# Kernel tuning notes

Hardware: AMD Instinct MI355X
Metric: run time of the kernel (lower is better)

Reference implementation:

```python
import jax, jax.numpy as jnp
import numpy as np

B, QS, KS, E, H = 2, 2048, 2048, 2048, 16
D = E // H  # head_dim = 128
EPS = 1e-6


def setup_inputs() -> dict:
    key = jax.random.key(0)
    ks = jax.random.split(key, 11)
    scale_in = 1.0 / np.sqrt(E)  # lecun_normal fan_in = E
    scale_out = 1.0 / np.sqrt(E)  # fan_in for out proj = H*D = E
    return {
        "q": jax.random.normal(ks[0], (B, QS, E), jnp.float32),
        "kv": jax.random.normal(ks[1], (B, KS, E), jnp.float32),
        "q_pos": jax.random.normal(ks[2], (B, QS, E), jnp.float32),
        "kv_pos": jax.random.normal(ks[3], (B, KS, E), jnp.float32),
        "mask": jax.random.bernoulli(ks[4], 0.5, (B, QS, KS)),
        "wq": jax.random.normal(ks[5], (E, H, D), jnp.float32) * scale_in,
        "wk": jax.random.normal(ks[6], (E, H, D), jnp.float32) * scale_in,
        "wv": jax.random.normal(ks[7], (E, H, D), jnp.float32) * scale_in,
        "q_ln_scale": jnp.ones((D,), jnp.float32),
        "k_ln_scale": jnp.ones((D,), jnp.float32),
        "wo": jax.random.normal(ks[8], (H, D, E), jnp.float32) * scale_out,
    }


def _layernorm_no_bias(x, scale):
    # flax LayerNorm over last axis, use_bias=False, epsilon=1e-6
    mu = jnp.mean(x, axis=-1, keepdims=True)
    var = jnp.mean(jnp.square(x - mu), axis=-1, keepdims=True)
    return (x - mu) * jax.lax.rsqrt(var + EPS) * scale


def reference(q, kv, q_pos, kv_pos, mask, wq, wk, wv, q_ln_scale, k_ln_scale, wo):
    dtype = q.dtype
    qi = q + q_pos          # [b, qs, e]
    ki = kv + kv_pos        # [b, ks, e]
    vi = kv
    # QKV projections (DenseGeneral, no bias) -> [b, s, h, d]
    qh = jnp.einsum('bqe,ehd->bqhd', qi, wq)
    kh = jnp.einsum('bke,ehd->bkhd', ki, wk)
    vh = jnp.einsum('bke,ehd->bkhd', vi, wv)
    # normalize_qk: LayerNorm (no bias) on query/key over head_dim
    qh = _layernorm_no_bias(qh, q_ln_scale)
    kh = _layernorm_no_bias(kh, k_ln_scale)
    # scaled dot-product with float32 logits
    qh = qh / jnp.sqrt(jnp.asarray(D, dtype))
    logits = jnp.einsum('bqhd,bkhd->bhqk', qh, kh,
                        preferred_element_type=jnp.float32)
    big_neg = jnp.finfo(jnp.float32).min
    logits = jnp.where(mask[:, None, :, :], logits, big_neg)
    attn = jax.nn.softmax(logits, axis=-1).astype(dtype)  # [b,h,q,k]
    out = jnp.einsum('bhqk,bkhd->bqhd', attn, vh)
    # output projection (DenseGeneral over (h,d), no bias)
    return jnp.einsum('bqhd,hde->bqe', out, wo)
```

## Files before the change

### kernel.cpp

```cpp
#include <hip/hip_runtime.h>
#include <hip/hip_bf16.h>


typedef __attribute__((ext_vector_type(8))) __bf16 bf16x8;
typedef __attribute__((ext_vector_type(4))) float f32x4;
typedef __attribute__((ext_vector_type(16))) float f32x16;
typedef __attribute__((ext_vector_type(8))) unsigned short ushort8;
typedef __attribute__((ext_vector_type(4))) unsigned short ushort4v;
typedef __attribute__((ext_vector_type(4))) unsigned uint4v;
typedef __attribute__((ext_vector_type(4))) float float4v;

#define MFMA16(a, b, c) __builtin_amdgcn_mfma_f32_16x16x32_bf16((a), (b), (c), 0, 0, 0)
#define MFMA32(a, b, c) __builtin_amdgcn_mfma_f32_32x32x16_bf16((a), (b), (c), 0, 0, 0)

__device__ __forceinline__ unsigned short f2bf(float f) {
  unsigned u = __builtin_bit_cast(unsigned, f);
  u += 0x7fffu + ((u >> 16) & 1u);
  return (unsigned short)(u >> 16);
}

__device__ __forceinline__ unsigned pkbf(float lo, float hi) {
  unsigned d;
  asm("v_cvt_pk_bf16_f32 %0, %1, %2" : "=v"(d) : "v"(lo), "v"(hi));
  return d;
}

__device__ __forceinline__ float max3f(float a, float b, float c) {
  float d;
  asm("v_max3_f32 %0, %1, %2, %3" : "=v"(d) : "v"(a), "v"(b), "v"(c));
  return d;
}

__device__ __forceinline__ float exp2a(float x) {
  float d;
  asm("v_exp_f32 %0, %1" : "=v"(d) : "v"(x));
  return d;
}

__device__ __forceinline__ void gload_lds16(const void* g, void* l) {
  __builtin_amdgcn_global_load_lds(
      (const __attribute__((address_space(1))) void*)g,
      (__attribute__((address_space(3))) void*)l, 16, 0, 0);
}

__global__ __launch_bounds__(256) void k_cvt(const float4v* __restrict__ x,
                                             const float4v* __restrict__ y,
                                             ushort4v* __restrict__ o, int n4) {
  int i = blockIdx.x * 256 + threadIdx.x;
  if (i >= n4) return;
  float4v a = x[i];
  if (y) { float4v b = y[i]; a = a + b; }
  ushort4v r;
  r[0] = f2bf(a[0]); r[1] = f2bf(a[1]); r[2] = f2bf(a[2]); r[3] = f2bf(a[3]);
  o[i] = r;
}

__global__ __launch_bounds__(256) void k_cvt2(const float4v* __restrict__ x,
                                              const float4v* __restrict__ y,
                                              ushort4v* __restrict__ oa,
                                              ushort4v* __restrict__ ob, int n4) {
  int i = blockIdx.x * 256 + threadIdx.x;
  if (i >= n4) return;
  float4v a = x[i];
  float4v s = a + y[i];
  ushort4v ra, rb;
  ra[0] = f2bf(s[0]); ra[1] = f2bf(s[1]); ra[2] = f2bf(s[2]); ra[3] = f2bf(s[3]);
  rb[0] = f2bf(a[0]); rb[1] = f2bf(a[1]); rb[2] = f2bf(a[2]); rb[3] = f2bf(a[3]);
  oa[i] = ra; ob[i] = rb;
}

__global__ __launch_bounds__(256) void k_tr(const float* __restrict__ s0, const float* __restrict__ s1,
                                            const float* __restrict__ s2, const float* __restrict__ s3,
                                            unsigned short* __restrict__ d0, unsigned short* __restrict__ d1,
                                            unsigned short* __restrict__ d2, unsigned short* __restrict__ d3) {
  __shared__ float t[32][33];
  const float* S; unsigned short* D;
  switch (blockIdx.z) {
    case 0: S = s0; D = d0; break;
    case 1: S = s1; D = d1; break;
    case 2: S = s2; D = d2; break;
    default: S = s3; D = d3; break;
  }
  int x = threadIdx.x & 31, y = threadIdx.x >> 5;
  int r0 = blockIdx.y * 32, c0 = blockIdx.x * 32;
#pragma unroll
  for (int i = 0; i < 4; ++i) t[y + 8 * i][x] = S[(size_t)(r0 + y + 8 * i) * 2048 + c0 + x];
  __syncthreads();
#pragma unroll
  for (int i = 0; i < 4; ++i)
    D[(size_t)(c0 + y + 8 * i) * 2048 + r0 + x] = f2bf(t[x][y + 8 * i]);
}

__global__ __launch_bounds__(256) void k_mask(const int* __restrict__ m,
                                              unsigned long long* __restrict__ out) {
  int i = blockIdx.x * 256 + threadIdx.x;
  unsigned long long b = __ballot(m[i] != 0);
  if ((threadIdx.x & 63) == 0) out[i >> 6] = b;
}

__global__ __launch_bounds__(256) void k_trv(const unsigned short* __restrict__ Vh,
                                             unsigned short* __restrict__ Vt) {
  __shared__ unsigned short t[64][72];
  int bh = blockIdx.z;
  int s0 = blockIdx.x * 64, d0 = blockIdx.y * 64;
  size_t base = (size_t)bh * 2048 * 128;
  int row = threadIdx.x >> 2, c16 = (threadIdx.x & 3) * 16;
  {
    const unsigned short* src = Vh + base + (size_t)(s0 + row) * 128 + d0 + c16;
    ushort8 a0 = *(const ushort8*)src;
    ushort8 a1 = *(const ushort8*)(src + 8);
#pragma unroll
    for (int e = 0; e < 8; ++e) {
      t[c16 + e][row] = a0[e];
      t[c16 + 8 + e][row] = a1[e];
    }
  }
  __syncthreads();
  {
    const int P0[8] = {0, 1, 2, 3, 8, 9, 10, 11};
    const int P1[8] = {4, 5, 6, 7, 12, 13, 14, 15};
    unsigned short* dst = Vt + base + (size_t)(d0 + row) * 2048 + s0 + c16;
    ushort8 w0, w1;
#pragma unroll
    for (int e = 0; e < 8; ++e) {
      w0[e] = t[row][c16 + P0[e]];
      w1[e] = t[row][c16 + P1[e]];
    }
    *(ushort8*)dst = w0;
    *(ushort8*)(dst + 8) = w1;
  }
}

template <int MODE>
__global__ __launch_bounds__(256) void k_gemm(const unsigned short* __restrict__ A,
                                              const unsigned short* __restrict__ Bt,
                                              void* __restrict__ Cv,
                                              const float* __restrict__ lnsc) {
  constexpr int K = 2048;
  __shared__ __attribute__((aligned(16))) unsigned short sA[128 * 64];
  __shared__ __attribute__((aligned(16))) unsigned short sB[128 * 64];
  __shared__ float sSum[2][128];
  __shared__ float sSq[2][128];
  int tid = threadIdx.x;
  int lane = tid & 63, w = tid >> 6;
  int wr = w >> 1, wc = w & 1;
  int r15 = lane & 15, blk = lane >> 4;
  int n0 = blockIdx.x * 128, m0 = blockIdx.y * 128;
  const unsigned short* Abase = A + (size_t)m0 * K;
  const unsigned short* Bbase = Bt + (size_t)n0 * K;
  f32x4 acc[4][4] = {};

  for (int kt = 0; kt < K; kt += 64) {
#pragma unroll
    for (int i = 0; i < 4; ++i) {
      int c = i * 256 + tid;
      int row = c >> 3, cc = c & 7;
      gload_lds16(Abase + (size_t)row * K + kt + ((cc ^ (row & 7)) * 8), &sA[c * 8]);
    }
#pragma unroll
    for (int i = 0; i < 4; ++i) {
      int c = i * 256 + tid;
      int row = c >> 3, cc = c & 7;
      gload_lds16(Bbase + (size_t)row * K + kt + ((cc ^ (row & 7)) * 8), &sB[c * 8]);
    }
    __syncthreads();
#pragma unroll
    for (int kk = 0; kk < 2; ++kk) {
      bf16x8 av[4], bv[4];
#pragma unroll
      for (int i = 0; i < 4; ++i) {
        int row = wr * 64 + i * 16 + r15;
        av[i] = *(const bf16x8*)&sA[row * 64 + (((kk * 4 + blk) ^ (row & 7)) * 8)];
      }
#pragma unroll
      for (int j = 0; j < 4; ++j) {
        int row = wc * 64 + j * 16 + r15;
        bv[j] = *(const bf16x8*)&sB[row * 64 + (((kk * 4 + blk) ^ (row & 7)) * 8)];
      }
#pragma unroll
      for (int i = 0; i < 4; ++i)
#pragma unroll
        for (int j = 0; j < 4; ++j) acc[i][j] = MFMA16(av[i], bv[j], acc[i][j]);
    }
    __syncthreads();
  }

  if constexpr (MODE == 3) {
    float* C = (float*)Cv;
#pragma unroll
    for (int i = 0; i < 4; ++i)
#pragma unroll
      for (int r = 0; r < 4; ++r)
#pragma unroll
        for (int j = 0; j < 4; ++j) {
          int rowl = wr * 64 + i * 16 + blk * 4 + r;
          int coll = wc * 64 + j * 16 + r15;
          C[(size_t)(m0 + rowl) * 2048 + n0 + coll] = acc[i][j][r];
        }
    return;
  } else {
    if constexpr (MODE == 1 || MODE == 2) {
#pragma unroll
      for (int i = 0; i < 4; ++i)
#pragma unroll
        for (int r = 0; r < 4; ++r) {
          float sm = 0.f, sq = 0.f;
#pragma unroll
          for (int j = 0; j < 4; ++j) { float v = acc[i][j][r]; sm += v; sq += v * v; }
          sm += __shfl_xor(sm, 1); sq += __shfl_xor(sq, 1);
          sm += __shfl_xor(sm, 2); sq += __shfl_xor(sq, 2);
          sm += __shfl_xor(sm, 4); sq += __shfl_xor(sq, 4);
          sm += __shfl_xor(sm, 8); sq += __shfl_xor(sq, 8);
          if (r15 == 0) {
            int rowl = wr * 64 + i * 16 + blk * 4 + r;
            sSum[wc][rowl] = sm; sSq[wc][rowl] = sq;
          }
        }
      __syncthreads();
    }
    unsigned short* Hout = (unsigned short*)Cv;
    int h = blockIdx.x;
#pragma unroll
    for (int i = 0; i < 4; ++i)
#pragma unroll
      for (int r = 0; r < 4; ++r) {
        int rowl = wr * 64 + i * 16 + blk * 4 + r;
        float mean = 0.f, rstd = 1.f;
        if constexpr (MODE == 1 || MODE == 2) {
          float sm = sSum[0][rowl] + sSum[1][rowl];
          float sq = sSq[0][rowl] + sSq[1][rowl];
          mean = sm * 0.0078125f;
          float var = sq * 0.0078125f - mean * mean;
          rstd = rsqrtf(var + 1e-6f);
        }
        int rowg = m0 + rowl;
        int b = rowg >> 11, s = rowg & 2047;
        unsigned short* orow = Hout + (((size_t)b * 16 + h) * 2048 + s) * 128;
#pragma unroll
        for (int j = 0; j < 4; ++j) {
          int d = wc * 64 + j * 16 + r15;
          float v = acc[i][j][r];
          if constexpr (MODE == 1)
            v = (v - mean) * rstd * lnsc[d] * (0.08838834764831845f * 1.4426950408889634f);
          if constexpr (MODE == 2) v = (v - mean) * rstd * lnsc[d];
          orow[d] = f2bf(v);
        }
      }
  }
}

__global__ __launch_bounds__(256, 2) void k_attn(const unsigned short* __restrict__ Qh,
                                                 const unsigned short* __restrict__ Kh,
                                                 const unsigned short* __restrict__ Vtp,
                                                 const unsigned* __restrict__ maskb,
                                                 unsigned short* __restrict__ O) {
  __shared__ __attribute__((aligned(16))) char smem[65536];
  int tid = threadIdx.x, w = tid >> 6;
  int lane = tid & 63;
  int q31 = lane & 31, hi = lane >> 5;
  int bh = blockIdx.y, b = bh >> 4, h = bh & 15;
  int qb = blockIdx.x * 128;
  size_t base = (size_t)bh * (2048 * 128);
  int qrow = qb + w * 32 + q31;

  bf16x8 qf[8];
  {
    const unsigned short* qp = Qh + base + (size_t)qrow * 128 + hi * 8;
#pragma unroll
    for (int wd = 0; wd < 8; ++wd) qf[wd] = *(const bf16x8*)(qp + wd * 16);
  }
  const unsigned* mrow = maskb + ((size_t)b * 2048 + qrow) * 64;

  const unsigned short* kgp[4];
  const unsigned short* vgp[4];
#pragma unroll
  for (int i = 0; i < 4; ++i) {
    int c = i * 256 + tid;
    int rr = c >> 4, cc = c & 15;
    kgp[i] = Kh + base + (size_t)rr * 128 + ((cc ^ (rr & 15)) * 8);
    int d = c >> 3, c8 = c & 7;
    vgp[i] = Vtp + base + (size_t)d * 2048 + ((c8 ^ (d & 7)) * 8);
  }

  f32x16 o[4] = {};
  float mv = -1e30f, ls = 0.f;

#pragma unroll
  for (int i = 0; i < 4; ++i) {
    int c = i * 256 + tid;
    gload_lds16(kgp[i], smem + c * 16);
    gload_lds16(vgp[i], smem + 16384 + c * 16);
  }
  __syncthreads();

  int cur = 0;
  for (int kc = 0; kc < 2048; kc += 64) {
    if (kc + 64 < 2048) {
      char* nb = smem + ((cur ^ 1) << 15);
#pragma unroll
      for (int i = 0; i < 4; ++i) {
        int c = i * 256 + tid;
        gload_lds16(kgp[i] + (size_t)(kc + 64) * 128, nb + c * 16);
        gload_lds16(vgp[i] + (kc + 64), nb + 16384 + c * 16);
      }
    }
    const unsigned short* sK = (const unsigned short*)(smem + (cur << 15));
    const unsigned short* sV = (const unsigned short*)(smem + (cur << 15) + 16384);

    unsigned mw0 = mrow[kc >> 5] >> (4 * hi);
    unsigned mw1 = mrow[(kc >> 5) + 1] >> (4 * hi);

    f32x16 st0 = {}, st1 = {};
#pragma unroll
    for (int wd = 0; wd < 8; ++wd) {
      int ck = ((2 * wd + hi) ^ (q31 & 15)) * 8;
      bf16x8 k0 = *(const bf16x8*)&sK[q31 * 128 + ck];
      bf16x8 k1 = *(const bf16x8*)&sK[(32 + q31) * 128 + ck];
      st0 = MFMA32(k0, qf[wd], st0);
      st1 = MFMA32(k1, qf[wd], st1);
    }

    float pvv[32];
#pragma unroll
    for (int r = 0; r < 16; ++r) {
      int bit = (r & 3) + 8 * (r >> 2);
      pvv[r] = ((mw0 >> bit) & 1u) ? st0[r] : -1e30f;
      pvv[16 + r] = ((mw1 >> bit) & 1u) ? st1[r] : -1e30f;
    }
    float c0 = max3f(pvv[0], pvv[1], pvv[2]);
    float c1 = max3f(pvv[3], pvv[4], pvv[5]);
    float c2 = max3f(pvv[6], pvv[7], pvv[8]);
    float c3 = max3f(pvv[9], pvv[10], pvv[11]);
    float c4 = max3f(pvv[12], pvv[13], pvv[14]);
    float c5 = max3f(pvv[15], pvv[16], pvv[17]);
    float c6 = max3f(pvv[18], pvv[19], pvv[20]);
    float c7 = max3f(pvv[21], pvv[22], pvv[23]);
    float c8 = max3f(pvv[24], pvv[25], pvv[26]);
    float c9 = max3f(pvv[27], pvv[28], pvv[29]);
    float ca = fmaxf(pvv[30], pvv[31]);
    float t0 = max3f(c0, c1, c2);
    float t1 = max3f(c3, c4, c5);
    float t2 = max3f(c6, c7, c8);
    float t3 = max3f(c9, ca, t0);
    float cmax = max3f(t1, t2, t3);
    cmax = fmaxf(cmax, __shfl_xor(cmax, 32));

    if (!__all(cmax - mv <= 11.5f)) {
      float mnew = fmaxf(mv, cmax);
      float fac = exp2a(mv - mnew);
      ls *= fac;
      float fr[16];
#pragma unroll
      for (int r = 0; r < 16; ++r) fr[r] = __shfl(fac, (r & 3) + 8 * (r >> 2) + 4 * hi);
#pragma unroll
      for (int dt = 0; dt < 4; ++dt)
#pragma unroll
        for (int r = 0; r < 16; ++r) o[dt][r] *= fr[r];
      mv = mnew;
    }

#pragma unroll
    for (int t = 0; t < 32; ++t) pvv[t] = exp2a(pvv[t] - mv);
    {
      float s0 = 0.f, s1 = 0.f, s2 = 0.f, s3 = 0.f;
#pragma unroll
      for (int t = 0; t < 8; ++t) {
        s0 += pvv[t]; s1 += pvv[8 + t]; s2 += pvv[16 + t]; s3 += pvv[24 + t];
      }
      ls += (s0 + s1) + (s2 + s3);
    }

    bf16x8 pa[4];
#pragma unroll
    for (int kw = 0; kw < 4; ++kw) {
      uint4v pw;
#pragma unroll
      for (int m = 0; m < 4; ++m) pw[m] = pkbf(pvv[8 * kw + 2 * m], pvv[8 * kw + 2 * m + 1]);
      pa[kw] = __builtin_bit_cast(bf16x8, pw);
    }

#pragma unroll
    for (int dt = 0; dt < 4; ++dt) {
      int vrow = dt * 32 + q31;
#pragma unroll
      for (int kw = 0; kw < 4; ++kw) {
        int cv = ((2 * kw + hi) ^ (q31 & 7)) * 8;
        bf16x8 vf = *(const bf16x8*)&sV[vrow * 64 + cv];
        o[dt] = MFMA32(pa[kw], vf, o[dt]);
      }
    }
    __syncthreads();
    cur ^= 1;
  }

  ls += __shfl_xor(ls, 32);
  float inv = 1.f / ls;
  float ir[16];
#pragma unroll
  for (int r = 0; r < 16; ++r) ir[r] = __shfl(inv, (r & 3) + 8 * (r >> 2) + 4 * hi);

  float* sO = (float*)smem;
#pragma unroll
  for (int pass = 0; pass < 2; ++pass) {
    __syncthreads();
    if ((w >> 1) == pass) {
      int wl = w & 1;
#pragma unroll
      for (int dt = 0; dt < 4; ++dt)
#pragma unroll
        for (int r = 0; r < 16; ++r) {
          int qrl = wl * 32 + (r & 3) + 8 * (r >> 2) + 4 * hi;
          sO[qrl * 132 + dt * 32 + q31] = o[dt][r] * ir[r];
        }
    }
    __syncthreads();
    {
      int row = tid >> 2, d0 = (tid & 3) * 32;
      int grow = qb + pass * 64 + row;
      unsigned short* op = O + (size_t)(b * 2048 + grow) * 2048 + h * 128 + d0;
#pragma unroll
      for (int g = 0; g < 4; ++g) {
        ushort8 pk;
#pragma unroll
        for (int e = 0; e < 8; ++e) pk[e] = f2bf(sO[row * 132 + d0 + g * 8 + e]);
        *(ushort8*)(op + g * 8) = pk;
      }
    }
  }
}

extern "C" void kernel_launch(void* const* d_in, const int* in_sizes, int n_in,
                              void* d_out, int out_size, void* d_ws, size_t ws_size,
                              hipStream_t stream) {
  const float* q      = (const float*)d_in[0];
  const float* kv     = (const float*)d_in[1];
  const float* q_pos  = (const float*)d_in[2];
  const float* kv_pos = (const float*)d_in[3];
  const int*   mask   = (const int*)d_in[4];
  const float* wq     = (const float*)d_in[5];
  const float* wk     = (const float*)d_in[6];
  const float* wv     = (const float*)d_in[7];
  const float* qls    = (const float*)d_in[8];
  const float* kls    = (const float*)d_in[9];
  const float* wo     = (const float*)d_in[10];

  char* ws = (char*)d_ws;
  const size_t SZ_ACT = (size_t)4096 * 2048 * 2;
  const size_t SZ_W   = (size_t)2048 * 2048 * 2;
  unsigned short* a_q = (unsigned short*)(ws);
  unsigned short* a_k = (unsigned short*)(ws + SZ_ACT);
  unsigned short* a_v = (unsigned short*)(ws + 2 * SZ_ACT);
  unsigned short* Qh  = (unsigned short*)(ws + 3 * SZ_ACT);
  unsigned short* Kh  = (unsigned short*)(ws + 4 * SZ_ACT);
  unsigned short* Vh  = (unsigned short*)(ws + 5 * SZ_ACT);
  unsigned short* wqt = (unsigned short*)(ws + 6 * SZ_ACT);
  unsigned short* wkt = (unsigned short*)(ws + 6 * SZ_ACT + SZ_W);
  unsigned short* wvt = (unsigned short*)(ws + 6 * SZ_ACT + 2 * SZ_W);
  unsigned short* wot = (unsigned short*)(ws + 6 * SZ_ACT + 3 * SZ_W);
  unsigned*       mkb = (unsigned*)(ws + 6 * SZ_ACT + 4 * SZ_W);
  unsigned short* Ob  = a_q;
  unsigned short* Vtr = a_k;

  const size_t NEED = 6 * SZ_ACT + 4 * SZ_W + (size_t)2 * 2048 * 64 * 4;
  if (ws_size < NEED) return;

  k_cvt<<<8192, 256, 0, stream>>>((const float4v*)q, (const float4v*)q_pos, (ushort4v*)a_q, 2097152);
  k_cvt2<<<8192, 256, 0, stream>>>((const float4v*)kv, (const float4v*)kv_pos,
                                   (ushort4v*)a_k, (ushort4v*)a_v, 2097152);
  k_tr<<<dim3(64, 64, 4), 256, 0, stream>>>(wq, wk, wv, wo, wqt, wkt, wvt, wot);
  k_mask<<<32768, 256, 0, stream>>>(mask, (unsigned long long*)mkb);

  k_gemm<1><<<dim3(16, 32), 256, 0, stream>>>(a_q, wqt, Qh, qls);
  k_gemm<2><<<dim3(16, 32), 256, 0, stream>>>(a_k, wkt, Kh, kls);
  k_gemm<0><<<dim3(16, 32), 256, 0, stream>>>(a_v, wvt, Vh, nullptr);

  k_trv<<<dim3(32, 2, 32), 256, 0, stream>>>(Vh, Vtr);

  k_attn<<<dim3(16, 32), 256, 0, stream>>>(Qh, Kh, Vtr, mkb, Ob);

  k_gemm<3><<<dim3(16, 32), 256, 0, stream>>>(Ob, wot, d_out, nullptr);
}
```

Before: 350.7 us.

## Compute V projection transposed directly, drop V transpose kernel, add MFMA priority hints

The V projection GEMM now runs with operands swapped (weights as A, activations as Bt), so it produces V^T directly. A new epilogue mode writes that result straight into the per-head transposed, permuted layout the attention kernel expects, which removes the separate k_trv transpose kernel and its extra global round trip. The attention kernel also raises wave priority around its two MFMA blocks using s_setprio. The risk is that the new epilogue writes with a scattered 16-element stride pattern, which may be less coalesced than the old row-major stores.

Result: faster. 339.3 us (-3.2%).

```diff
diff --git a/kernel.cpp b/kernel.cpp
--- a/kernel.cpp
+++ b/kernel.cpp
@@ -96,39 +96,6 @@
   int i = blockIdx.x * 256 + threadIdx.x;
   unsigned long long b = __ballot(m[i] != 0);
   if ((threadIdx.x & 63) == 0) out[i >> 6] = b;
-}
-
-__global__ __launch_bounds__(256) void k_trv(const unsigned short* __restrict__ Vh,
-                                             unsigned short* __restrict__ Vt) {
-  __shared__ unsigned short t[64][72];
-  int bh = blockIdx.z;
-  int s0 = blockIdx.x * 64, d0 = blockIdx.y * 64;
-  size_t base = (size_t)bh * 2048 * 128;
-  int row = threadIdx.x >> 2, c16 = (threadIdx.x & 3) * 16;
-  {
-    const unsigned short* src = Vh + base + (size_t)(s0 + row) * 128 + d0 + c16;
-    ushort8 a0 = *(const ushort8*)src;
-    ushort8 a1 = *(const ushort8*)(src + 8);
-#pragma unroll
-    for (int e = 0; e < 8; ++e) {
-      t[c16 + e][row] = a0[e];
-      t[c16 + 8 + e][row] = a1[e];
-    }
-  }
-  __syncthreads();
-  {
-    const int P0[8] = {0, 1, 2, 3, 8, 9, 10, 11};
-    const int P1[8] = {4, 5, 6, 7, 12, 13, 14, 15};
-    unsigned short* dst = Vt + base + (size_t)(d0 + row) * 2048 + s0 + c16;
-    ushort8 w0, w1;
-#pragma unroll
-    for (int e = 0; e < 8; ++e) {
-      w0[e] = t[row][c16 + P0[e]];
-      w1[e] = t[row][c16 + P1[e]];
-    }
-    *(ushort8*)dst = w0;
-    *(ushort8*)(dst + 8) = w1;
-  }
 }
 
 template <int MODE>
@@ -198,6 +165,23 @@
           C[(size_t)(m0 + rowl) * 2048 + n0 + coll] = acc[i][j][r];
         }
     return;
+  } else if constexpr (MODE == 4) {
+    unsigned short* Vtp = (unsigned short*)Cv;
+    int p15 = (r15 & 3) | ((r15 & 4) << 1) | ((r15 & 8) >> 1);
+#pragma unroll
+    for (int i = 0; i < 4; ++i)
+#pragma unroll
+      for (int r = 0; r < 4; ++r) {
+        int rowg = m0 + wr * 64 + i * 16 + blk * 4 + r;
+        int h = rowg >> 7, d = rowg & 127;
+#pragma unroll
+        for (int j = 0; j < 4; ++j) {
+          int col = n0 + wc * 64 + j * 16;
+          int b = col >> 11, s16 = col & 2047;
+          Vtp[(((size_t)(b * 16 + h) * 128 + d) * 2048) + s16 + p15] = f2bf(acc[i][j][r]);
+        }
+      }
+    return;
   } else {
     if constexpr (MODE == 1 || MODE == 2) {
 #pragma unroll
@@ -311,6 +295,7 @@
     unsigned mw1 = mrow[(kc >> 5) + 1] >> (4 * hi);
 
     f32x16 st0 = {}, st1 = {};
+    __builtin_amdgcn_s_setprio(1);
 #pragma unroll
     for (int wd = 0; wd < 8; ++wd) {
       int ck = ((2 * wd + hi) ^ (q31 & 15)) * 8;
@@ -319,6 +304,7 @@
       st0 = MFMA32(k0, qf[wd], st0);
       st1 = MFMA32(k1, qf[wd], st1);
     }
+    __builtin_amdgcn_s_setprio(0);
 
     float pvv[32];
 #pragma unroll
@@ -379,6 +365,7 @@
       pa[kw] = __builtin_bit_cast(bf16x8, pw);
     }
 
+    __builtin_amdgcn_s_setprio(1);
 #pragma unroll
     for (int dt = 0; dt < 4; ++dt) {
       int vrow = dt * 32 + q31;
@@ -389,6 +376,7 @@
         o[dt] = MFMA32(pa[kw], vf, o[dt]);
       }
     }
+    __builtin_amdgcn_s_setprio(0);
     __syncthreads();
     cur ^= 1;
   }
@@ -452,14 +440,13 @@
   unsigned short* a_v = (unsigned short*)(ws + 2 * SZ_ACT);
   unsigned short* Qh  = (unsigned short*)(ws + 3 * SZ_ACT);
   unsigned short* Kh  = (unsigned short*)(ws + 4 * SZ_ACT);
-  unsigned short* Vh  = (unsigned short*)(ws + 5 * SZ_ACT);
   unsigned short* wqt = (unsigned short*)(ws + 6 * SZ_ACT);
   unsigned short* wkt = (unsigned short*)(ws + 6 * SZ_ACT + SZ_W);
   unsigned short* wvt = (unsigned short*)(ws + 6 * SZ_ACT + 2 * SZ_W);
   unsigned short* wot = (unsigned short*)(ws + 6 * SZ_ACT + 3 * SZ_W);
   unsigned*       mkb = (unsigned*)(ws + 6 * SZ_ACT + 4 * SZ_W);
   unsigned short* Ob  = a_q;
-  unsigned short* Vtr = a_k;
+  unsigned short* Vtr = (unsigned short*)(ws + 5 * SZ_ACT);
 
   const size_t NEED = 6 * SZ_ACT + 4 * SZ_W + (size_t)2 * 2048 * 64 * 4;
   if (ws_size < NEED) return;
@@ -472,9 +459,7 @@
 
   k_gemm<1><<<dim3(16, 32), 256, 0, stream>>>(a_q, wqt, Qh, qls);
   k_gemm<2><<<dim3(16, 32), 256, 0, stream>>>(a_k, wkt, Kh, kls);
-  k_gemm<0><<<dim3(16, 32), 256, 0, stream>>>(a_v, wvt, Vh, nullptr);
-
-  k_trv<<<dim3(32, 2, 32), 256, 0, stream>>>(Vh, Vtr);
+  k_gemm<4><<<dim3(32, 16), 256, 0, stream>>>(wvt, a_v, Vtr, nullptr);
 
   k_attn<<<dim3(16, 32), 256, 0, stream>>>(Qh, Kh, Vtr, mkb, Ob);
 
```
